# Optimization experiments

Measured on AMD Instinct MI355X. Metric: run time of the kernel, lower is better.

## Reference

```python
import jax, jax.numpy as jnp
import numpy as np

N_NODES = 100000
N_EDGES = 1600000
N_GRAPHS = 1024
D_IN = 128
D_HID = 128
D_OUT = 2


def setup_inputs() -> dict:
    key = jax.random.key(0)
    ks = jax.random.split(key, 12)
    x = jax.random.normal(ks[0], (N_NODES, D_IN), dtype=jnp.float32)
    edge_index = jax.random.randint(ks[1], (2, N_EDGES), 0, N_NODES, dtype=jnp.int32)
    batch = jnp.sort(jax.random.randint(ks[2], (N_NODES,), 0, N_GRAPHS, dtype=jnp.int32))
    def lin(k, fan_in, fan_out):
        bound = 1.0 / np.sqrt(fan_in)
        kw, kb = jax.random.split(k)
        W = jax.random.uniform(kw, (fan_in, fan_out), minval=-bound, maxval=bound, dtype=jnp.float32)
        b = jax.random.uniform(kb, (fan_out,), minval=-bound, maxval=bound, dtype=jnp.float32)
        return W, b
    W1, b1 = lin(ks[3], D_IN, D_HID)
    W2, b2 = lin(ks[4], D_HID, D_HID)
    fc1_w, fc1_b = lin(ks[5], D_HID, D_HID)
    fc2_w, fc2_b = lin(ks[6], D_HID, D_OUT)
    return {"x": x, "edge_index": edge_index, "batch": batch,
            "W1": W1, "b1": b1, "W2": W2, "b2": b2,
            "fc1_w": fc1_w, "fc1_b": fc1_b, "fc2_w": fc2_w, "fc2_b": fc2_b}


def gcn_conv(x, W, b, src, dst, deg_inv_sqrt, n_nodes):
    # GCNConv: out = D^-1/2 (A + I) D^-1/2 (x W) + b, using edge list with self-loops
    h = x @ W  # [N, d_out]
    norm = deg_inv_sqrt[src] * deg_inv_sqrt[dst]  # [E+N]
    msg = h[src] * norm[:, None]  # gather + scale
    out = jnp.zeros((n_nodes, h.shape[1]), dtype=h.dtype).at[dst].add(msg)
    return out + b


def reference(x, edge_index, batch, W1, b1, W2, b2, fc1_w, fc1_b, fc2_w, fc2_b):
    n = x.shape[0]
    loops = jnp.arange(n, dtype=edge_index.dtype)
    src = jnp.concatenate([edge_index[0], loops])  # add self-loops (PyG default)
    dst = jnp.concatenate([edge_index[1], loops])
    deg = jnp.zeros((n,), dtype=x.dtype).at[dst].add(1.0)
    deg_inv_sqrt = jax.lax.rsqrt(deg)  # deg >= 1 due to self-loops

    h = jax.nn.relu(gcn_conv(x, W1, b1, src, dst, deg_inv_sqrt, n))
    # dropout p=0.5 is identity in eval mode
    h = jax.nn.relu(gcn_conv(h, W2, b2, src, dst, deg_inv_sqrt, n))

    # global_mean_pool over batch assignment
    sums = jax.ops.segment_sum(h, batch, num_segments=N_GRAPHS)
    cnts = jax.ops.segment_sum(jnp.ones((n,), dtype=h.dtype), batch, num_segments=N_GRAPHS)
    pooled = sums / jnp.maximum(cnts, 1.0)[:, None]  # [G, d]

    g = jax.nn.relu(pooled @ fc1_w + fc1_b)
    logits = g @ fc2_w + fc2_b
    return jax.nn.log_softmax(logits, axis=1)
```

## Files before the change

kernel.cpp:

```cpp
#include <hip/hip_runtime.h>
#include <hip/hip_fp16.h>
#include <math.h>


#define D_FEAT 128
#define BSHIFT 9
#define BNODES 512
#define CHUNK 4096
#define CAPB 16384

using half8   = __attribute__((ext_vector_type(8))) _Float16;
using half4   = __attribute__((ext_vector_type(4))) _Float16;
using floatx4 = __attribute__((ext_vector_type(4))) float;
using floatx2 = __attribute__((ext_vector_type(2))) float;

__global__ void __launch_bounds__(256) binA_kernel(const int* __restrict__ edges,
                                                   int* __restrict__ gcur,
                                                   int* __restrict__ binned, int E, int nb) {
    __shared__ int h[256];
    __shared__ int cur[256];
    __shared__ int base[256];
    int t = threadIdx.x;
    int c0 = blockIdx.x * CHUNK;
    int sv[CHUNK / 256], bv[CHUNK / 256];
    int i0 = c0 + t * (CHUNK / 256);
    if (i0 + (CHUNK / 256) <= E) {
#pragma unroll
        for (int k = 0; k < CHUNK / 256; k += 4) {
            int4 s4 = *(const int4*)&edges[i0 + k];
            int4 d4 = *(const int4*)&edges[E + i0 + k];
            bv[k + 0] = d4.x >> BSHIFT; sv[k + 0] = ((d4.x & (BNODES - 1)) << 17) | s4.x;
            bv[k + 1] = d4.y >> BSHIFT; sv[k + 1] = ((d4.y & (BNODES - 1)) << 17) | s4.y;
            bv[k + 2] = d4.z >> BSHIFT; sv[k + 2] = ((d4.z & (BNODES - 1)) << 17) | s4.z;
            bv[k + 3] = d4.w >> BSHIFT; sv[k + 3] = ((d4.w & (BNODES - 1)) << 17) | s4.w;
        }
    } else {
#pragma unroll
        for (int k = 0; k < CHUNK / 256; ++k) {
            int i = i0 + k;
            if (i < E) {
                int s = edges[i], d = edges[E + i];
                bv[k] = d >> BSHIFT;
                sv[k] = ((d & (BNODES - 1)) << 17) | s;
            } else bv[k] = -1;
        }
    }
    h[t] = 0;
    __syncthreads();
#pragma unroll
    for (int k = 0; k < CHUNK / 256; ++k)
        if (bv[k] >= 0) atomicAdd(&h[bv[k]], 1);
    __syncthreads();
    if (t < nb && h[t] > 0) base[t] = atomicAdd(&gcur[t], h[t]);
    cur[t] = 0;
    __syncthreads();
#pragma unroll
    for (int k = 0; k < CHUNK / 256; ++k)
        if (bv[k] >= 0) {
            int b = bv[k];
            int r = atomicAdd(&cur[b], 1);
            int pos = base[b] + r;
            if (pos < CAPB) binned[b * CAPB + pos] = sv[k];
        }
}

__global__ void bucket_scan_kernel(const int* __restrict__ gcur, int* __restrict__ bucketBase,
                                   int nb, int E) {
    __shared__ int sdata[256];
    int t = threadIdx.x;
    int v = (t < nb) ? gcur[t] : 0;
    sdata[t] = v;
    __syncthreads();
    for (int d = 1; d < 256; d <<= 1) {
        int u = (t >= d) ? sdata[t - d] : 0;
        __syncthreads();
        sdata[t] += u;
        __syncthreads();
    }
    if (t < nb) bucketBase[t] = sdata[t] - v;
    if (t == 0) bucketBase[nb] = E;
}

__global__ void __launch_bounds__(256) binB1_kernel(const int* __restrict__ binned,
                                                    const int* __restrict__ bucketBase,
                                                    const int* __restrict__ gcur,
                                                    float* __restrict__ dis,
                                                    int* __restrict__ rowptr,
                                                    int* __restrict__ gcursor,
                                                    int N, int E, int nb) {
    __shared__ int hist[BNODES];
    __shared__ int sdata[256];
    int t = threadIdx.x;
    int b = blockIdx.x;
    int node0 = b << BSHIFT;
    int e0 = bucketBase[b];
    int cnt = gcur[b];
    const int* bin = binned + (size_t)b * CAPB;
    hist[t] = 0; hist[t + 256] = 0;
    __syncthreads();
    for (int i = t; i < cnt; i += 256) atomicAdd(&hist[bin[i] >> 17], 1);
    __syncthreads();
    int a0 = hist[2 * t], a1 = hist[2 * t + 1];
    int pair = a0 + a1;
    sdata[t] = pair;
    __syncthreads();
    for (int d = 1; d < 256; d <<= 1) {
        int u = (t >= d) ? sdata[t - d] : 0;
        __syncthreads();
        sdata[t] += u;
        __syncthreads();
    }
    int excl = sdata[t] - pair;
    int p0 = e0 + excl, p1 = e0 + excl + a0;
    gcursor[(b << BSHIFT) + 2 * t] = p0;
    gcursor[(b << BSHIFT) + 2 * t + 1] = p1;
    int n0 = node0 + 2 * t, n1 = node0 + 2 * t + 1;
    if (n0 < N) { rowptr[n0] = p0; dis[n0] = rsqrtf((float)a0 + 1.0f); }
    if (n1 < N) { rowptr[n1] = p1; dis[n1] = rsqrtf((float)a1 + 1.0f); }
    if (b == nb - 1 && t == 0) rowptr[N] = E;
}

__global__ void __launch_bounds__(256) binB2_kernel(const int* __restrict__ binned,
                                                    const int* __restrict__ gcur,
                                                    const int* __restrict__ gcursor,
                                                    const float* __restrict__ dis,
                                                    int2* __restrict__ csr,
                                                    int N, int nb) {
    __shared__ int cur[BNODES];
    __shared__ float dloc[BNODES];
    int t = threadIdx.x;
    int b = blockIdx.x;
    int node0 = b << BSHIFT;
    int cnt = gcur[b];
    const int* bin = binned + (size_t)b * CAPB;
#pragma unroll
    for (int i = 0; i < 2; ++i) {
        int idx = t + i * 256;
        cur[idx] = gcursor[(b << BSHIFT) + idx];
        int n = node0 + idx;
        dloc[idx] = (n < N) ? dis[n] : 0.f;
    }
    __syncthreads();
    for (int i = t; i < cnt; i += 256) {
        int v = bin[i];
        int dstl = v >> 17, s = v & 0x1FFFF;
        int p = atomicAdd(&cur[dstl], 1);
        float nrm = dis[s] * dloc[dstl];
        csr[p] = make_int2(s, __float_as_int(nrm));
    }
}

__global__ void wprep_kernel(const float* __restrict__ W1, const float* __restrict__ W2,
                             _Float16* __restrict__ Wt1, _Float16* __restrict__ Wt2) {
    int i = blockIdx.x * blockDim.x + threadIdx.x;
    int n = i >> 7, k = i & 127;
    Wt1[i] = (_Float16)W1[k * 128 + n];
    Wt2[i] = (_Float16)W2[k * 128 + n];
}

template <bool HALF_IN>
__global__ void __launch_bounds__(256) gemm_mfma_kernel(const void* __restrict__ Xv,
                                                        const _Float16* __restrict__ WtG,
                                                        unsigned char* __restrict__ Y8, int N) {
    __shared__ _Float16 wt[128][136];
    int t = threadIdx.x;
    int row0 = blockIdx.x * 64;

#pragma unroll
    for (int i = 0; i < 8; ++i) {
        int c = t + i * 256;
        int r = c >> 4, c8 = (c & 15) * 8;
        *(half8*)&wt[r][c8] = *(const half8*)&WtG[r * 128 + c8];
    }

    int wave = t >> 6, lane = t & 63;
    int m = lane & 15, quad = lane >> 4;
    int grow = row0 + wave * 16 + m;

    half8 a[4];
    if (grow < N) {
        if (HALF_IN) {
            const _Float16* Xp = (const _Float16*)Xv;
#pragma unroll
            for (int k = 0; k < 4; ++k)
                a[k] = *(const half8*)&Xp[(size_t)grow * 128 + k * 32 + quad * 8];
        } else {
            const float* Xp = (const float*)Xv;
#pragma unroll
            for (int k = 0; k < 4; ++k) {
                float4 v0 = *(const float4*)&Xp[(size_t)grow * 128 + k * 32 + quad * 8];
                float4 v1 = *(const float4*)&Xp[(size_t)grow * 128 + k * 32 + quad * 8 + 4];
                a[k] = (half8){(_Float16)v0.x, (_Float16)v0.y, (_Float16)v0.z, (_Float16)v0.w,
                               (_Float16)v1.x, (_Float16)v1.y, (_Float16)v1.z, (_Float16)v1.w};
            }
        }
    } else {
#pragma unroll
        for (int k = 0; k < 4; ++k) a[k] = (half8){};
    }
    __syncthreads();

    floatx4 acc[8];
#pragma unroll
    for (int nt = 0; nt < 8; ++nt) acc[nt] = (floatx4){0.f, 0.f, 0.f, 0.f};
#pragma unroll
    for (int nt = 0; nt < 8; ++nt) {
#pragma unroll
        for (int k = 0; k < 4; ++k) {
            half8 bfr = *(const half8*)&wt[nt * 16 + m][k * 32 + quad * 8];
            acc[nt] = __builtin_amdgcn_mfma_f32_16x16x32_f16(a[k], bfr, acc[nt], 0, 0, 0);
        }
    }
#pragma unroll
    for (int nt = 0; nt < 8; ++nt) {
#pragma unroll
        for (int r = 0; r < 4; ++r) {
            int row = row0 + wave * 16 + quad * 4 + r;
            if (row < N) {
                float v = acc[nt][r];
                unsigned char q =
                    (unsigned char)(__builtin_amdgcn_cvt_pk_fp8_f32(v, v, 0, false) & 0xff);
                Y8[(size_t)row * 128 + nt * 16 + m] = q;
            }
        }
    }
}

__global__ void __launch_bounds__(256) agg_kernel(const unsigned char* __restrict__ H8,
                                                  const int* __restrict__ rowptr,
                                                  const int2* __restrict__ csr,
                                                  const float* __restrict__ dis,
                                                  const float* __restrict__ bias,
                                                  _Float16* __restrict__ out, int N) {
    int v = (blockIdx.x * blockDim.x + threadIdx.x) >> 6;
    int lane = threadIdx.x & 63;
    if (v >= N) return;
    int half = lane >> 5, sl = lane & 31;
    int r0 = __builtin_amdgcn_readfirstlane(rowptr[v]);
    int r1 = __builtin_amdgcn_readfirstlane(rowptr[v + 1]);
    float dv = __builtin_amdgcn_readfirstlane(__float_as_int(dis[v]));
    dv = __int_as_float(__float_as_int(dv));
    unsigned fo = (unsigned)(sl << 2);

    floatx2 a01, a23;
    {
        float wself = 0.5f * __int_as_float(__builtin_amdgcn_readfirstlane(
                          __float_as_int(dis[v] * dis[v])));
        unsigned int u = *(const unsigned int*)(H8 + (((unsigned)v << 7) | fo));
        floatx2 lo = __builtin_amdgcn_cvt_pk_f32_fp8(u, false);
        floatx2 hi = __builtin_amdgcn_cvt_pk_f32_fp8(u, true);
        floatx2 w2 = {wself, wself};
        a01 = w2 * lo;
        a23 = w2 * hi;
    }
#define ACC(uu, ww)                                                     \
        {                                                               \
            floatx2 lo = __builtin_amdgcn_cvt_pk_f32_fp8(uu, false);    \
            floatx2 hi = __builtin_amdgcn_cvt_pk_f32_fp8(uu, true);     \
            floatx2 w2 = {(ww), (ww)};                                  \
            a01 += w2 * lo;                                             \
            a23 += w2 * hi;                                             \
        }
    int e = r0 + half;
    for (; e + 14 < r1; e += 16) {
        int2 c0 = csr[e],      c1 = csr[e + 2],  c2 = csr[e + 4],  c3 = csr[e + 6];
        int2 c4 = csr[e + 8],  c5 = csr[e + 10], c6 = csr[e + 12], c7 = csr[e + 14];
        unsigned int u0 = *(const unsigned int*)(H8 + (((unsigned)c0.x << 7) | fo));
        unsigned int u1 = *(const unsigned int*)(H8 + (((unsigned)c1.x << 7) | fo));
        unsigned int u2 = *(const unsigned int*)(H8 + (((unsigned)c2.x << 7) | fo));
        unsigned int u3 = *(const unsigned int*)(H8 + (((unsigned)c3.x << 7) | fo));
        unsigned int u4 = *(const unsigned int*)(H8 + (((unsigned)c4.x << 7) | fo));
        unsigned int u5 = *(const unsigned int*)(H8 + (((unsigned)c5.x << 7) | fo));
        unsigned int u6 = *(const unsigned int*)(H8 + (((unsigned)c6.x << 7) | fo));
        unsigned int u7 = *(const unsigned int*)(H8 + (((unsigned)c7.x << 7) | fo));
        ACC(u0, __int_as_float(c0.y)) ACC(u1, __int_as_float(c1.y))
        ACC(u2, __int_as_float(c2.y)) ACC(u3, __int_as_float(c3.y))
        ACC(u4, __int_as_float(c4.y)) ACC(u5, __int_as_float(c5.y))
        ACC(u6, __int_as_float(c6.y)) ACC(u7, __int_as_float(c7.y))
    }
    if (e < r1) {
        int last = r1 - 1;
        int2 cc[8];
        unsigned int uu[8];
        float ww[8];
#pragma unroll
        for (int k = 0; k < 8; ++k) {
            int idx = e + 2 * k;
            cc[k] = csr[idx < last ? idx : last];
            ww[k] = (idx < r1) ? __int_as_float(cc[k].y) : 0.f;
        }
#pragma unroll
        for (int k = 0; k < 8; ++k)
            uu[k] = *(const unsigned int*)(H8 + (((unsigned)cc[k].x << 7) | fo));
#pragma unroll
        for (int k = 0; k < 8; ++k) ACC(uu[k], ww[k])
    }
#undef ACC
    a01[0] += __shfl_xor(a01[0], 32, 64);
    a01[1] += __shfl_xor(a01[1], 32, 64);
    a23[0] += __shfl_xor(a23[0], 32, 64);
    a23[1] += __shfl_xor(a23[1], 32, 64);
    if (half == 0) {
        float4 b = *(const float4*)&bias[sl * 4];
        half4 o = {(_Float16)fmaxf(a01[0] + b.x, 0.f), (_Float16)fmaxf(a01[1] + b.y, 0.f),
                   (_Float16)fmaxf(a23[0] + b.z, 0.f), (_Float16)fmaxf(a23[1] + b.w, 0.f)};
        *(half4*)&out[(size_t)v * 128 + sl * 4] = o;
    }
}

__device__ __forceinline__ int lower_bound_i(const int* a, int n, int key) {
    int lo = 0, hi = n;
    while (lo < hi) {
        int mid = (lo + hi) >> 1;
        if (a[mid] < key) lo = mid + 1;
        else hi = mid;
    }
    return lo;
}

__global__ void __launch_bounds__(512) pool_kernel(const _Float16* __restrict__ H,
                                                   const int* __restrict__ batch,
                                                   float* __restrict__ pooled, int N) {
    __shared__ int range[2];
    __shared__ float part[4][128];
    int g = blockIdx.x;
    int t = threadIdx.x;
    int j = t & 127, rg = t >> 7;
    if (t < 2) range[t] = lower_bound_i(batch, N, g + t);
    __syncthreads();
    int lo = range[0], hi = range[1];
    float s = 0.f;
    for (int v = lo + rg; v < hi; v += 4) s += (float)H[(size_t)v * 128 + j];
    part[rg][j] = s;
    __syncthreads();
    if (rg == 0) {
        float tot = part[0][j] + part[1][j] + part[2][j] + part[3][j];
        pooled[g * 128 + j] = tot / fmaxf((float)(hi - lo), 1.0f);
    }
}

__global__ void head_kernel(const float* __restrict__ pooled, const float* __restrict__ fc1w,
                            const float* __restrict__ fc1b, const float* __restrict__ fc2w,
                            const float* __restrict__ fc2b, float* __restrict__ out) {
    __shared__ float p[128];
    __shared__ float r0[128], r1[128];
    int g = blockIdx.x;
    int j = threadIdx.x;
    p[j] = pooled[g * 128 + j];
    __syncthreads();
    float acc = fc1b[j];
#pragma unroll 8
    for (int k = 0; k < 128; ++k) acc = fmaf(p[k], fc1w[k * 128 + j], acc);
    float gv = fmaxf(acc, 0.f);
    r0[j] = gv * fc2w[j * 2 + 0];
    r1[j] = gv * fc2w[j * 2 + 1];
    __syncthreads();
    for (int s = 64; s > 0; s >>= 1) {
        if (j < s) {
            r0[j] += r0[j + s];
            r1[j] += r1[j + s];
        }
        __syncthreads();
    }
    if (j == 0) {
        float l0 = r0[0] + fc2b[0];
        float l1 = r1[0] + fc2b[1];
        float m = fmaxf(l0, l1);
        float lse = m + logf(expf(l0 - m) + expf(l1 - m));
        out[g * 2 + 0] = l0 - lse;
        out[g * 2 + 1] = l1 - lse;
    }
}

extern "C" void kernel_launch(void* const* d_in, const int* in_sizes, int n_in,
                              void* d_out, int out_size, void* d_ws, size_t ws_size,
                              hipStream_t stream) {
    const float* x    = (const float*)d_in[0];
    const int* edges  = (const int*)d_in[1];
    const int* batch  = (const int*)d_in[2];
    const float* W1   = (const float*)d_in[3];
    const float* b1   = (const float*)d_in[4];
    const float* W2   = (const float*)d_in[5];
    const float* b2   = (const float*)d_in[6];
    const float* fc1w = (const float*)d_in[7];
    const float* fc1b = (const float*)d_in[8];
    const float* fc2w = (const float*)d_in[9];
    const float* fc2b = (const float*)d_in[10];
    float* out = (float*)d_out;

    int N = in_sizes[2];
    int E = in_sizes[1] / 2;
    int G = out_size / 2;
    int nb = (N + BNODES - 1) / BNODES;
    int nA = (E + CHUNK - 1) / CHUNK;

    char* ws = (char*)d_ws;
    size_t off = 0;
    auto alloc = [&](size_t bytes) -> char* {
        char* ptr = ws + off;
        off += (bytes + 255) & ~(size_t)255;
        return ptr;
    };
    int* gcur          = (int*)alloc((size_t)nb * 4);
    int* bucketBase    = (int*)alloc((size_t)(nb + 1) * 4);
    int* binned        = (int*)alloc((size_t)nb * CAPB * 4);
    int* rowptr        = (int*)alloc((size_t)(N + 1) * 4);
    float* dis         = (float*)alloc((size_t)N * 4);
    int* gcursor       = (int*)alloc((size_t)nb * BNODES * 4);
    int2* csr          = (int2*)alloc((size_t)E * 8);
    _Float16* Wt1      = (_Float16*)alloc(128 * 128 * 2);
    _Float16* Wt2      = (_Float16*)alloc(128 * 128 * 2);
    unsigned char* buf8 = (unsigned char*)alloc((size_t)N * D_FEAT);
    _Float16* bufH     = (_Float16*)alloc((size_t)N * D_FEAT * 2);
    float* pooled      = (float*)alloc((size_t)G * D_FEAT * 4);

    hipMemsetAsync(gcur, 0, (size_t)nb * 4, stream);

    binA_kernel<<<nA, 256, 0, stream>>>(edges, gcur, binned, E, nb);
    bucket_scan_kernel<<<1, 256, 0, stream>>>(gcur, bucketBase, nb, E);
    binB1_kernel<<<nb, 256, 0, stream>>>(binned, bucketBase, gcur, dis, rowptr, gcursor, N, E, nb);
    binB2_kernel<<<nb, 256, 0, stream>>>(binned, gcur, gcursor, dis, csr, N, nb);
    wprep_kernel<<<64, 256, 0, stream>>>(W1, W2, Wt1, Wt2);

    const int tb = 256;
    int gAgg = (N * 64 + tb - 1) / tb;
    int gGemm = (N + 63) / 64;
    gemm_mfma_kernel<false><<<gGemm, 256, 0, stream>>>((const void*)x, Wt1, buf8, N);
    agg_kernel<<<gAgg, tb, 0, stream>>>(buf8, rowptr, csr, dis, b1, bufH, N);
    gemm_mfma_kernel<true><<<gGemm, 256, 0, stream>>>((const void*)bufH, Wt2, buf8, N);
    agg_kernel<<<gAgg, tb, 0, stream>>>(buf8, rowptr, csr, dis, b2, bufH, N);
    pool_kernel<<<G, 512, 0, stream>>>(bufH, batch, pooled, N);
    head_kernel<<<G, 128, 0, stream>>>(pooled, fc1w, fc1b, fc2w, fc2b, out);
}
```

Before: 300.5 us.

## Split each node's aggregation across two waves and fold bucket scan into binB1

The aggregation kernel now assigns two wavefronts per node. Each wave handles an interleaved quarter-stride of the edge list with a 4-deep unroll, and the partial sums are combined through shared memory before the bias, ReLU and store. The self-loop weight is halved to 0.25 per wave so the two copies add up correctly. The separate single-block bucket scan kernel is removed, and each binB1 block recomputes the prefix sum over bucket counts itself. This cuts one launch and aims at more memory-level parallelism per node, at the cost of a block barrier, shared-memory traffic and less unrolling per wave.

```diff
diff --git a/kernel.cpp b/kernel.cpp
--- a/kernel.cpp
+++ b/kernel.cpp
@@ -64,25 +64,7 @@
         }
 }
 
-__global__ void bucket_scan_kernel(const int* __restrict__ gcur, int* __restrict__ bucketBase,
-                                   int nb, int E) {
-    __shared__ int sdata[256];
-    int t = threadIdx.x;
-    int v = (t < nb) ? gcur[t] : 0;
-    sdata[t] = v;
-    __syncthreads();
-    for (int d = 1; d < 256; d <<= 1) {
-        int u = (t >= d) ? sdata[t - d] : 0;
-        __syncthreads();
-        sdata[t] += u;
-        __syncthreads();
-    }
-    if (t < nb) bucketBase[t] = sdata[t] - v;
-    if (t == 0) bucketBase[nb] = E;
-}
-
 __global__ void __launch_bounds__(256) binB1_kernel(const int* __restrict__ binned,
-                                                    const int* __restrict__ bucketBase,
                                                     const int* __restrict__ gcur,
                                                     float* __restrict__ dis,
                                                     int* __restrict__ rowptr,
@@ -93,8 +75,18 @@
     int t = threadIdx.x;
     int b = blockIdx.x;
     int node0 = b << BSHIFT;
-    int e0 = bucketBase[b];
     int cnt = gcur[b];
+    int gval = (t < nb) ? gcur[t] : 0;
+    sdata[t] = gval;
+    __syncthreads();
+    for (int d = 1; d < 256; d <<= 1) {
+        int u = (t >= d) ? sdata[t - d] : 0;
+        __syncthreads();
+        sdata[t] += u;
+        __syncthreads();
+    }
+    int e0 = sdata[b] - cnt;
+    __syncthreads();
     const int* bin = binned + (size_t)b * CAPB;
     hist[t] = 0; hist[t + 256] = 0;
     __syncthreads();
@@ -232,27 +224,30 @@
                                                   const float* __restrict__ dis,
                                                   const float* __restrict__ bias,
                                                   _Float16* __restrict__ out, int N) {
-    int v = (blockIdx.x * blockDim.x + threadIdx.x) >> 6;
-    int lane = threadIdx.x & 63;
-    if (v >= N) return;
+    __shared__ float4 part[64];
+    int t = threadIdx.x;
+    int wave = t >> 6, lane = t & 63;
+    int nd = wave >> 1, wv = wave & 1;
+    int v = blockIdx.x * 2 + nd;
     int half = lane >> 5, sl = lane & 31;
-    int r0 = __builtin_amdgcn_readfirstlane(rowptr[v]);
-    int r1 = __builtin_amdgcn_readfirstlane(rowptr[v + 1]);
-    float dv = __builtin_amdgcn_readfirstlane(__float_as_int(dis[v]));
-    dv = __int_as_float(__float_as_int(dv));
+    bool valid = (v < N);
     unsigned fo = (unsigned)(sl << 2);
 
-    floatx2 a01, a23;
-    {
-        float wself = 0.5f * __int_as_float(__builtin_amdgcn_readfirstlane(
-                          __float_as_int(dis[v] * dis[v])));
-        unsigned int u = *(const unsigned int*)(H8 + (((unsigned)v << 7) | fo));
-        floatx2 lo = __builtin_amdgcn_cvt_pk_f32_fp8(u, false);
-        floatx2 hi = __builtin_amdgcn_cvt_pk_f32_fp8(u, true);
-        floatx2 w2 = {wself, wself};
-        a01 = w2 * lo;
-        a23 = w2 * hi;
-    }
+    floatx2 a01 = {0.f, 0.f}, a23 = {0.f, 0.f};
+    int r0 = 0, r1 = 0;
+    if (valid) {
+        r0 = rowptr[v];
+        r1 = rowptr[v + 1];
+        float dv = dis[v];
+        {
+            float wself = 0.25f * dv * dv;
+            unsigned int u = *(const unsigned int*)(H8 + (((unsigned)v << 7) | fo));
+            floatx2 lo = __builtin_amdgcn_cvt_pk_f32_fp8(u, false);
+            floatx2 hi = __builtin_amdgcn_cvt_pk_f32_fp8(u, true);
+            floatx2 w2 = {wself, wself};
+            a01 = w2 * lo;
+            a23 = w2 * hi;
+        }
 #define ACC(uu, ww)                                                     \
         {                                                               \
             floatx2 lo = __builtin_amdgcn_cvt_pk_f32_fp8(uu, false);    \
@@ -261,49 +256,49 @@
             a01 += w2 * lo;                                             \
             a23 += w2 * hi;                                             \
         }
-    int e = r0 + half;
-    for (; e + 14 < r1; e += 16) {
-        int2 c0 = csr[e],      c1 = csr[e + 2],  c2 = csr[e + 4],  c3 = csr[e + 6];
-        int2 c4 = csr[e + 8],  c5 = csr[e + 10], c6 = csr[e + 12], c7 = csr[e + 14];
-        unsigned int u0 = *(const unsigned int*)(H8 + (((unsigned)c0.x << 7) | fo));
-        unsigned int u1 = *(const unsigned int*)(H8 + (((unsigned)c1.x << 7) | fo));
-        unsigned int u2 = *(const unsigned int*)(H8 + (((unsigned)c2.x << 7) | fo));
-        unsigned int u3 = *(const unsigned int*)(H8 + (((unsigned)c3.x << 7) | fo));
-        unsigned int u4 = *(const unsigned int*)(H8 + (((unsigned)c4.x << 7) | fo));
-        unsigned int u5 = *(const unsigned int*)(H8 + (((unsigned)c5.x << 7) | fo));
-        unsigned int u6 = *(const unsigned int*)(H8 + (((unsigned)c6.x << 7) | fo));
-        unsigned int u7 = *(const unsigned int*)(H8 + (((unsigned)c7.x << 7) | fo));
-        ACC(u0, __int_as_float(c0.y)) ACC(u1, __int_as_float(c1.y))
-        ACC(u2, __int_as_float(c2.y)) ACC(u3, __int_as_float(c3.y))
-        ACC(u4, __int_as_float(c4.y)) ACC(u5, __int_as_float(c5.y))
-        ACC(u6, __int_as_float(c6.y)) ACC(u7, __int_as_float(c7.y))
-    }
-    if (e < r1) {
-        int last = r1 - 1;
-        int2 cc[8];
-        unsigned int uu[8];
-        float ww[8];
-#pragma unroll
-        for (int k = 0; k < 8; ++k) {
-            int idx = e + 2 * k;
-            cc[k] = csr[idx < last ? idx : last];
-            ww[k] = (idx < r1) ? __int_as_float(cc[k].y) : 0.f;
-        }
-#pragma unroll
-        for (int k = 0; k < 8; ++k)
-            uu[k] = *(const unsigned int*)(H8 + (((unsigned)cc[k].x << 7) | fo));
-#pragma unroll
-        for (int k = 0; k < 8; ++k) ACC(uu[k], ww[k])
-    }
+        int e = r0 + wv * 2 + half;
+        for (; e + 12 < r1; e += 16) {
+            int2 c0 = csr[e], c1 = csr[e + 4], c2 = csr[e + 8], c3 = csr[e + 12];
+            unsigned int u0 = *(const unsigned int*)(H8 + (((unsigned)c0.x << 7) | fo));
+            unsigned int u1 = *(const unsigned int*)(H8 + (((unsigned)c1.x << 7) | fo));
+            unsigned int u2 = *(const unsigned int*)(H8 + (((unsigned)c2.x << 7) | fo));
+            unsigned int u3 = *(const unsigned int*)(H8 + (((unsigned)c3.x << 7) | fo));
+            ACC(u0, __int_as_float(c0.y)) ACC(u1, __int_as_float(c1.y))
+            ACC(u2, __int_as_float(c2.y)) ACC(u3, __int_as_float(c3.y))
+        }
+        if (e < r1) {
+            int last = r1 - 1;
+            int2 cc[4];
+            unsigned int uu[4];
+            float ww[4];
+#pragma unroll
+            for (int k = 0; k < 4; ++k) {
+                int idx = e + 4 * k;
+                cc[k] = csr[idx < last ? idx : last];
+                ww[k] = (idx < r1) ? __int_as_float(cc[k].y) : 0.f;
+            }
+#pragma unroll
+            for (int k = 0; k < 4; ++k)
+                uu[k] = *(const unsigned int*)(H8 + (((unsigned)cc[k].x << 7) | fo));
+#pragma unroll
+            for (int k = 0; k < 4; ++k) ACC(uu[k], ww[k])
+        }
 #undef ACC
-    a01[0] += __shfl_xor(a01[0], 32, 64);
-    a01[1] += __shfl_xor(a01[1], 32, 64);
-    a23[0] += __shfl_xor(a23[0], 32, 64);
-    a23[1] += __shfl_xor(a23[1], 32, 64);
-    if (half == 0) {
+        a01[0] += __shfl_xor(a01[0], 32, 64);
+        a01[1] += __shfl_xor(a01[1], 32, 64);
+        a23[0] += __shfl_xor(a23[0], 32, 64);
+        a23[1] += __shfl_xor(a23[1], 32, 64);
+    }
+    if (valid && wv == 1 && half == 0)
+        part[nd * 32 + sl] = make_float4(a01[0], a01[1], a23[0], a23[1]);
+    __syncthreads();
+    if (valid && wv == 0 && half == 0) {
+        float4 p = part[nd * 32 + sl];
         float4 b = *(const float4*)&bias[sl * 4];
-        half4 o = {(_Float16)fmaxf(a01[0] + b.x, 0.f), (_Float16)fmaxf(a01[1] + b.y, 0.f),
-                   (_Float16)fmaxf(a23[0] + b.z, 0.f), (_Float16)fmaxf(a23[1] + b.w, 0.f)};
+        half4 o = {(_Float16)fmaxf(a01[0] + p.x + b.x, 0.f),
+                   (_Float16)fmaxf(a01[1] + p.y + b.y, 0.f),
+                   (_Float16)fmaxf(a23[0] + p.z + b.z, 0.f),
+                   (_Float16)fmaxf(a23[1] + p.w + b.w, 0.f)};
         *(half4*)&out[(size_t)v * 128 + sl * 4] = o;
     }
 }
@@ -402,7 +397,6 @@
         return ptr;
     };
     int* gcur          = (int*)alloc((size_t)nb * 4);
-    int* bucketBase    = (int*)alloc((size_t)(nb + 1) * 4);
     int* binned        = (int*)alloc((size_t)nb * CAPB * 4);
     int* rowptr        = (int*)alloc((size_t)(N + 1) * 4);
     float* dis         = (float*)alloc((size_t)N * 4);
@@ -417,18 +411,16 @@
     hipMemsetAsync(gcur, 0, (size_t)nb * 4, stream);
 
     binA_kernel<<<nA, 256, 0, stream>>>(edges, gcur, binned, E, nb);
-    bucket_scan_kernel<<<1, 256, 0, stream>>>(gcur, bucketBase, nb, E);
-    binB1_kernel<<<nb, 256, 0, stream>>>(binned, bucketBase, gcur, dis, rowptr, gcursor, N, E, nb);
+    binB1_kernel<<<nb, 256, 0, stream>>>(binned, gcur, dis, rowptr, gcursor, N, E, nb);
     binB2_kernel<<<nb, 256, 0, stream>>>(binned, gcur, gcursor, dis, csr, N, nb);
     wprep_kernel<<<64, 256, 0, stream>>>(W1, W2, Wt1, Wt2);
 
-    const int tb = 256;
-    int gAgg = (N * 64 + tb - 1) / tb;
+    int gAgg = (N + 1) / 2;
     int gGemm = (N + 63) / 64;
     gemm_mfma_kernel<false><<<gGemm, 256, 0, stream>>>((const void*)x, Wt1, buf8, N);
-    agg_kernel<<<gAgg, tb, 0, stream>>>(buf8, rowptr, csr, dis, b1, bufH, N);
+    agg_kernel<<<gAgg, 256, 0, stream>>>(buf8, rowptr, csr, dis, b1, bufH, N);
     gemm_mfma_kernel<true><<<gGemm, 256, 0, stream>>>((const void*)bufH, Wt2, buf8, N);
-    agg_kernel<<<gAgg, tb, 0, stream>>>(buf8, rowptr, csr, dis, b2, bufH, N);
+    agg_kernel<<<gAgg, 256, 0, stream>>>(buf8, rowptr, csr, dis, b2, bufH, N);
     pool_kernel<<<G, 512, 0, stream>>>(bufH, batch, pooled, N);
     head_kernel<<<G, 128, 0, stream>>>(pooled, fc1w, fc1b, fc2w, fc2b, out);
 }
```

After: 334.7 us. +11.4%, slower.

## Factor GCN edge norm into GEMM epilogue and agg output, store src-only CSR

Applied to the files above, without the earlier changes.

Splits the symmetric normalization: the source-side deg^-1/2 is applied to each row in the GEMM epilogue before fp8 quantization, and the destination-side factor is applied once per node after aggregation. The CSR then holds only 4-byte source indices instead of (src, weight) pairs, which halves edge-list traffic in both aggregation passes and removes the dis gather from binB2. The separate bucket scan kernel is also folded into binB1, with every block redundantly scanning the bucket counts to drop one launch. The fp8 quantization now applies to pre-scaled values, which slightly changes rounding behaviour.

```diff
diff --git a/kernel.cpp b/kernel.cpp
--- a/kernel.cpp
+++ b/kernel.cpp
@@ -64,25 +64,7 @@
         }
 }
 
-__global__ void bucket_scan_kernel(const int* __restrict__ gcur, int* __restrict__ bucketBase,
-                                   int nb, int E) {
-    __shared__ int sdata[256];
-    int t = threadIdx.x;
-    int v = (t < nb) ? gcur[t] : 0;
-    sdata[t] = v;
-    __syncthreads();
-    for (int d = 1; d < 256; d <<= 1) {
-        int u = (t >= d) ? sdata[t - d] : 0;
-        __syncthreads();
-        sdata[t] += u;
-        __syncthreads();
-    }
-    if (t < nb) bucketBase[t] = sdata[t] - v;
-    if (t == 0) bucketBase[nb] = E;
-}
-
 __global__ void __launch_bounds__(256) binB1_kernel(const int* __restrict__ binned,
-                                                    const int* __restrict__ bucketBase,
                                                     const int* __restrict__ gcur,
                                                     float* __restrict__ dis,
                                                     int* __restrict__ rowptr,
@@ -93,8 +75,18 @@
     int t = threadIdx.x;
     int b = blockIdx.x;
     int node0 = b << BSHIFT;
-    int e0 = bucketBase[b];
     int cnt = gcur[b];
+    int gval = (t < nb) ? gcur[t] : 0;
+    sdata[t] = gval;
+    __syncthreads();
+    for (int d = 1; d < 256; d <<= 1) {
+        int u = (t >= d) ? sdata[t - d] : 0;
+        __syncthreads();
+        sdata[t] += u;
+        __syncthreads();
+    }
+    int e0 = sdata[b] - cnt;
+    __syncthreads();
     const int* bin = binned + (size_t)b * CAPB;
     hist[t] = 0; hist[t + 256] = 0;
     __syncthreads();
@@ -123,30 +115,19 @@
 __global__ void __launch_bounds__(256) binB2_kernel(const int* __restrict__ binned,
                                                     const int* __restrict__ gcur,
                                                     const int* __restrict__ gcursor,
-                                                    const float* __restrict__ dis,
-                                                    int2* __restrict__ csr,
-                                                    int N, int nb) {
+                                                    int* __restrict__ csr, int nb) {
     __shared__ int cur[BNODES];
-    __shared__ float dloc[BNODES];
     int t = threadIdx.x;
     int b = blockIdx.x;
-    int node0 = b << BSHIFT;
     int cnt = gcur[b];
     const int* bin = binned + (size_t)b * CAPB;
-#pragma unroll
-    for (int i = 0; i < 2; ++i) {
-        int idx = t + i * 256;
-        cur[idx] = gcursor[(b << BSHIFT) + idx];
-        int n = node0 + idx;
-        dloc[idx] = (n < N) ? dis[n] : 0.f;
-    }
+    cur[t] = gcursor[(b << BSHIFT) + t];
+    cur[t + 256] = gcursor[(b << BSHIFT) + t + 256];
     __syncthreads();
     for (int i = t; i < cnt; i += 256) {
         int v = bin[i];
-        int dstl = v >> 17, s = v & 0x1FFFF;
-        int p = atomicAdd(&cur[dstl], 1);
-        float nrm = dis[s] * dloc[dstl];
-        csr[p] = make_int2(s, __float_as_int(nrm));
+        int p = atomicAdd(&cur[v >> 17], 1);
+        csr[p] = v & 0x1FFFF;
     }
 }
 
@@ -161,6 +142,7 @@
 template <bool HALF_IN>
 __global__ void __launch_bounds__(256) gemm_mfma_kernel(const void* __restrict__ Xv,
                                                         const _Float16* __restrict__ WtG,
+                                                        const float* __restrict__ dis,
                                                         unsigned char* __restrict__ Y8, int N) {
     __shared__ _Float16 wt[128][136];
     int t = threadIdx.x;
@@ -211,13 +193,15 @@
             acc[nt] = __builtin_amdgcn_mfma_f32_16x16x32_f16(a[k], bfr, acc[nt], 0, 0, 0);
         }
     }
-#pragma unroll
-    for (int nt = 0; nt < 8; ++nt) {
-#pragma unroll
-        for (int r = 0; r < 4; ++r) {
-            int row = row0 + wave * 16 + quad * 4 + r;
-            if (row < N) {
-                float v = acc[nt][r];
+    int orow = row0 + wave * 16 + quad * 4;
+#pragma unroll
+    for (int r = 0; r < 4; ++r) {
+        int row = orow + r;
+        if (row < N) {
+            float dr = dis[row];
+#pragma unroll
+            for (int nt = 0; nt < 8; ++nt) {
+                float v = acc[nt][r] * dr;
                 unsigned char q =
                     (unsigned char)(__builtin_amdgcn_cvt_pk_fp8_f32(v, v, 0, false) & 0xff);
                 Y8[(size_t)row * 128 + nt * 16 + m] = q;
@@ -228,7 +212,7 @@
 
 __global__ void __launch_bounds__(256) agg_kernel(const unsigned char* __restrict__ H8,
                                                   const int* __restrict__ rowptr,
-                                                  const int2* __restrict__ csr,
+                                                  const int* __restrict__ csr,
                                                   const float* __restrict__ dis,
                                                   const float* __restrict__ bias,
                                                   _Float16* __restrict__ out, int N) {
@@ -236,74 +220,73 @@
     int lane = threadIdx.x & 63;
     if (v >= N) return;
     int half = lane >> 5, sl = lane & 31;
-    int r0 = __builtin_amdgcn_readfirstlane(rowptr[v]);
-    int r1 = __builtin_amdgcn_readfirstlane(rowptr[v + 1]);
-    float dv = __builtin_amdgcn_readfirstlane(__float_as_int(dis[v]));
-    dv = __int_as_float(__float_as_int(dv));
+    int r0 = rowptr[v], r1 = rowptr[v + 1];
+    float dv = dis[v];
     unsigned fo = (unsigned)(sl << 2);
 
     floatx2 a01, a23;
     {
-        float wself = 0.5f * __int_as_float(__builtin_amdgcn_readfirstlane(
-                          __float_as_int(dis[v] * dis[v])));
         unsigned int u = *(const unsigned int*)(H8 + (((unsigned)v << 7) | fo));
         floatx2 lo = __builtin_amdgcn_cvt_pk_f32_fp8(u, false);
         floatx2 hi = __builtin_amdgcn_cvt_pk_f32_fp8(u, true);
-        floatx2 w2 = {wself, wself};
-        a01 = w2 * lo;
-        a23 = w2 * hi;
-    }
-#define ACC(uu, ww)                                                     \
+        floatx2 hf = {0.5f, 0.5f};
+        a01 = hf * lo;
+        a23 = hf * hi;
+    }
+#define ACC(uu)                                                         \
         {                                                               \
-            floatx2 lo = __builtin_amdgcn_cvt_pk_f32_fp8(uu, false);    \
-            floatx2 hi = __builtin_amdgcn_cvt_pk_f32_fp8(uu, true);     \
+            a01 += __builtin_amdgcn_cvt_pk_f32_fp8(uu, false);          \
+            a23 += __builtin_amdgcn_cvt_pk_f32_fp8(uu, true);           \
+        }
+#define ACCW(uu, ww)                                                    \
+        {                                                               \
             floatx2 w2 = {(ww), (ww)};                                  \
-            a01 += w2 * lo;                                             \
-            a23 += w2 * hi;                                             \
+            a01 += w2 * __builtin_amdgcn_cvt_pk_f32_fp8(uu, false);     \
+            a23 += w2 * __builtin_amdgcn_cvt_pk_f32_fp8(uu, true);      \
         }
     int e = r0 + half;
     for (; e + 14 < r1; e += 16) {
-        int2 c0 = csr[e],      c1 = csr[e + 2],  c2 = csr[e + 4],  c3 = csr[e + 6];
-        int2 c4 = csr[e + 8],  c5 = csr[e + 10], c6 = csr[e + 12], c7 = csr[e + 14];
-        unsigned int u0 = *(const unsigned int*)(H8 + (((unsigned)c0.x << 7) | fo));
-        unsigned int u1 = *(const unsigned int*)(H8 + (((unsigned)c1.x << 7) | fo));
-        unsigned int u2 = *(const unsigned int*)(H8 + (((unsigned)c2.x << 7) | fo));
-        unsigned int u3 = *(const unsigned int*)(H8 + (((unsigned)c3.x << 7) | fo));
-        unsigned int u4 = *(const unsigned int*)(H8 + (((unsigned)c4.x << 7) | fo));
-        unsigned int u5 = *(const unsigned int*)(H8 + (((unsigned)c5.x << 7) | fo));
-        unsigned int u6 = *(const unsigned int*)(H8 + (((unsigned)c6.x << 7) | fo));
-        unsigned int u7 = *(const unsigned int*)(H8 + (((unsigned)c7.x << 7) | fo));
-        ACC(u0, __int_as_float(c0.y)) ACC(u1, __int_as_float(c1.y))
-        ACC(u2, __int_as_float(c2.y)) ACC(u3, __int_as_float(c3.y))
-        ACC(u4, __int_as_float(c4.y)) ACC(u5, __int_as_float(c5.y))
-        ACC(u6, __int_as_float(c6.y)) ACC(u7, __int_as_float(c7.y))
+        int s0 = csr[e],      s1 = csr[e + 2],  s2 = csr[e + 4],  s3 = csr[e + 6];
+        int s4 = csr[e + 8],  s5 = csr[e + 10], s6 = csr[e + 12], s7 = csr[e + 14];
+        unsigned int u0 = *(const unsigned int*)(H8 + (((unsigned)s0 << 7) | fo));
+        unsigned int u1 = *(const unsigned int*)(H8 + (((unsigned)s1 << 7) | fo));
+        unsigned int u2 = *(const unsigned int*)(H8 + (((unsigned)s2 << 7) | fo));
+        unsigned int u3 = *(const unsigned int*)(H8 + (((unsigned)s3 << 7) | fo));
+        unsigned int u4 = *(const unsigned int*)(H8 + (((unsigned)s4 << 7) | fo));
+        unsigned int u5 = *(const unsigned int*)(H8 + (((unsigned)s5 << 7) | fo));
+        unsigned int u6 = *(const unsigned int*)(H8 + (((unsigned)s6 << 7) | fo));
+        unsigned int u7 = *(const unsigned int*)(H8 + (((unsigned)s7 << 7) | fo));
+        ACC(u0) ACC(u1) ACC(u2) ACC(u3) ACC(u4) ACC(u5) ACC(u6) ACC(u7)
     }
     if (e < r1) {
         int last = r1 - 1;
-        int2 cc[8];
+        int ss[8];
         unsigned int uu[8];
         float ww[8];
 #pragma unroll
         for (int k = 0; k < 8; ++k) {
             int idx = e + 2 * k;
-            cc[k] = csr[idx < last ? idx : last];
-            ww[k] = (idx < r1) ? __int_as_float(cc[k].y) : 0.f;
+            ss[k] = csr[idx < last ? idx : last];
+            ww[k] = (idx < r1) ? 1.f : 0.f;
         }
 #pragma unroll
         for (int k = 0; k < 8; ++k)
-            uu[k] = *(const unsigned int*)(H8 + (((unsigned)cc[k].x << 7) | fo));
-#pragma unroll
-        for (int k = 0; k < 8; ++k) ACC(uu[k], ww[k])
+            uu[k] = *(const unsigned int*)(H8 + (((unsigned)ss[k] << 7) | fo));
+#pragma unroll
+        for (int k = 0; k < 8; ++k) ACCW(uu[k], ww[k])
     }
 #undef ACC
+#undef ACCW
     a01[0] += __shfl_xor(a01[0], 32, 64);
     a01[1] += __shfl_xor(a01[1], 32, 64);
     a23[0] += __shfl_xor(a23[0], 32, 64);
     a23[1] += __shfl_xor(a23[1], 32, 64);
     if (half == 0) {
         float4 b = *(const float4*)&bias[sl * 4];
-        half4 o = {(_Float16)fmaxf(a01[0] + b.x, 0.f), (_Float16)fmaxf(a01[1] + b.y, 0.f),
-                   (_Float16)fmaxf(a23[0] + b.z, 0.f), (_Float16)fmaxf(a23[1] + b.w, 0.f)};
+        half4 o = {(_Float16)fmaxf(dv * a01[0] + b.x, 0.f),
+                   (_Float16)fmaxf(dv * a01[1] + b.y, 0.f),
+                   (_Float16)fmaxf(dv * a23[0] + b.z, 0.f),
+                   (_Float16)fmaxf(dv * a23[1] + b.w, 0.f)};
         *(half4*)&out[(size_t)v * 128 + sl * 4] = o;
     }
 }
@@ -402,12 +385,11 @@
         return ptr;
     };
     int* gcur          = (int*)alloc((size_t)nb * 4);
-    int* bucketBase    = (int*)alloc((size_t)(nb + 1) * 4);
     int* binned        = (int*)alloc((size_t)nb * CAPB * 4);
     int* rowptr        = (int*)alloc((size_t)(N + 1) * 4);
     float* dis         = (float*)alloc((size_t)N * 4);
     int* gcursor       = (int*)alloc((size_t)nb * BNODES * 4);
-    int2* csr          = (int2*)alloc((size_t)E * 8);
+    int* csr           = (int*)alloc((size_t)E * 4);
     _Float16* Wt1      = (_Float16*)alloc(128 * 128 * 2);
     _Float16* Wt2      = (_Float16*)alloc(128 * 128 * 2);
     unsigned char* buf8 = (unsigned char*)alloc((size_t)N * D_FEAT);
@@ -417,18 +399,16 @@
     hipMemsetAsync(gcur, 0, (size_t)nb * 4, stream);
 
     binA_kernel<<<nA, 256, 0, stream>>>(edges, gcur, binned, E, nb);
-    bucket_scan_kernel<<<1, 256, 0, stream>>>(gcur, bucketBase, nb, E);
-    binB1_kernel<<<nb, 256, 0, stream>>>(binned, bucketBase, gcur, dis, rowptr, gcursor, N, E, nb);
-    binB2_kernel<<<nb, 256, 0, stream>>>(binned, gcur, gcursor, dis, csr, N, nb);
+    binB1_kernel<<<nb, 256, 0, stream>>>(binned, gcur, dis, rowptr, gcursor, N, E, nb);
+    binB2_kernel<<<nb, 256, 0, stream>>>(binned, gcur, gcursor, csr, nb);
     wprep_kernel<<<64, 256, 0, stream>>>(W1, W2, Wt1, Wt2);
 
-    const int tb = 256;
-    int gAgg = (N * 64 + tb - 1) / tb;
+    int gAgg = (N * 64 + 255) / 256;
     int gGemm = (N + 63) / 64;
-    gemm_mfma_kernel<false><<<gGemm, 256, 0, stream>>>((const void*)x, Wt1, buf8, N);
-    agg_kernel<<<gAgg, tb, 0, stream>>>(buf8, rowptr, csr, dis, b1, bufH, N);
-    gemm_mfma_kernel<true><<<gGemm, 256, 0, stream>>>((const void*)bufH, Wt2, buf8, N);
-    agg_kernel<<<gAgg, tb, 0, stream>>>(buf8, rowptr, csr, dis, b2, bufH, N);
+    gemm_mfma_kernel<false><<<gGemm, 256, 0, stream>>>((const void*)x, Wt1, dis, buf8, N);
+    agg_kernel<<<gAgg, 256, 0, stream>>>(buf8, rowptr, csr, dis, b1, bufH, N);
+    gemm_mfma_kernel<true><<<gGemm, 256, 0, stream>>>((const void*)bufH, Wt2, dis, buf8, N);
+    agg_kernel<<<gAgg, 256, 0, stream>>>(buf8, rowptr, csr, dis, b2, bufH, N);
     pool_kernel<<<G, 512, 0, stream>>>(bufH, batch, pooled, N);
     head_kernel<<<G, 128, 0, stream>>>(pooled, fc1w, fc1b, fc2w, fc2b, out);
 }
```

Measured after the change: 282.0 us. 6.2% less time.
